# Kernel tuning notes

Hardware: AMD Instinct MI355X
Metric: run time of the kernel (lower is better)

The kernel has to match this reference:

```python
import jax, jax.numpy as jnp
import numpy as np

ALPHA = 0.2          # LeakyReLU negative slope
NEG = -9e15          # mask fill value, as in pyGAT GraphAttentionLayer
N, NIN, NHID, NOUT = 4096, 64, 32, 64
NHEADS, D_INT = 8, 32
H_INT = max(1, int(NHEADS * 0.25))   # 2 intent heads
H_SP = NHEADS - H_INT                # 6 spatial heads


def setup_inputs() -> dict:
    key = jax.random.key(0)
    ks = jax.random.split(key, 10)
    x = jax.random.normal(ks[0], (N, NIN), dtype=jnp.float32)
    adj = (jax.random.uniform(ks[1], (N, N)) < 0.01).astype(jnp.float32)
    adj = jnp.clip(adj + jnp.eye(N, dtype=jnp.float32), 0.0, 1.0)
    intent_embeds = jax.random.normal(ks[2], (N, D_INT), dtype=jnp.float32)
    # learned params (xavier-ish scale)
    def xav(k, shape):
        fan = shape[-2] if len(shape) > 1 else shape[-1]
        return jax.random.normal(k, shape, dtype=jnp.float32) / np.sqrt(fan)
    W_sp = xav(ks[3], (H_SP, NIN, NHID))       # spatial head projections
    a_sp = xav(ks[4], (H_SP, 2 * NHID))        # spatial attention vectors
    W_int = xav(ks[5], (H_INT, NIN, NHID))     # intent head projections
    a_int = xav(ks[6], (H_INT, 2 * D_INT))     # intent attention vectors (over intent embeds)
    W_out = xav(ks[7], (NHID * NHEADS, NOUT))  # output GAT layer
    a_out = xav(ks[8], (2 * NOUT,))
    return {"x": x, "adj": adj, "intent_embeds": intent_embeds,
            "W_sp": W_sp, "a_sp": a_sp, "W_int": W_int, "a_int": a_int,
            "W_out": W_out, "a_out": a_out}


def _masked_attend(e, mask, Wh):
    # e: [H,N,N] raw scores, mask: [1,N,N] bool, Wh: [H,N,F]
    att = jax.nn.softmax(jnp.where(mask, e, NEG), axis=-1)
    return jnp.einsum('hij,hjf->hif', att, Wh)


def reference(x, adj, intent_embeds, W_sp, a_sp, W_int, a_int, W_out, a_out):
    mask = (adj > 0)[None]                                   # [1,N,N]
    # ---- spatial heads (standard GAT, batched over heads) ----
    Wh_s = jnp.einsum('nf,hfo->hno', x, W_sp)                # [Hs,N,nhid]
    f1 = jnp.einsum('hno,ho->hn', Wh_s, a_sp[:, :NHID])
    f2 = jnp.einsum('hno,ho->hn', Wh_s, a_sp[:, NHID:])
    e_s = jax.nn.leaky_relu(f1[:, :, None] + f2[:, None, :], ALPHA)
    h_s = jax.nn.elu(_masked_attend(e_s, mask, Wh_s))        # concat=True -> elu
    # ---- intent heads: scores from intent embeddings, values from Wh ----
    Wh_i = jnp.einsum('nf,hfo->hno', x, W_int)               # [Hi,N,nhid]
    g1 = jnp.einsum('nd,hd->hn', intent_embeds, a_int[:, :D_INT])
    g2 = jnp.einsum('nd,hd->hn', intent_embeds, a_int[:, D_INT:])
    e_i = jax.nn.leaky_relu(g1[:, :, None] + g2[:, None, :], ALPHA)
    h_i = jax.nn.elu(_masked_attend(e_i, mask, Wh_i))        # [Hi,N,nhid]
    # ---- concat heads along feature dim: [N, nheads*nhid] ----
    h = jnp.concatenate([h_s, h_i], axis=0).transpose(1, 0, 2).reshape(N, -1)
    # ---- output attention layer (concat=False: no elu) ----
    Who = h @ W_out                                          # [N,nout]
    o1 = Who @ a_out[:NOUT]
    o2 = Who @ a_out[NOUT:]
    e_o = jax.nn.leaky_relu(o1[:, None] + o2[None, :], ALPHA)
    att_o = jax.nn.softmax(jnp.where(mask[0], e_o, NEG), axis=-1)
    out = att_o @ Who
    return jnp.tanh(out)
```

## Files before the change

kernel.cpp:

```cpp
#include <hip/hip_runtime.h>

#define N      4096
#define NIN    64
#define NHID   32
#define NOUT   64
#define NHEADS 8
#define H_SP   6
#define D_INT  32
#define MAXDEG 128
#define NPB    4
#define NPB2   2
#define ALPHA  0.2f

__device__ __forceinline__ int mbcnt64(unsigned long long m) {
    return __builtin_amdgcn_mbcnt_hi((unsigned)(m >> 32),
           __builtin_amdgcn_mbcnt_lo((unsigned)m, 0u));
}

__global__ __launch_bounds__(256) void k_fused1(
    const float* __restrict__ x, const float* __restrict__ ie,
    const float4* __restrict__ adj4,
    const float* __restrict__ Wsp, const float* __restrict__ asp,
    const float* __restrict__ Wint, const float* __restrict__ aint,
    float* __restrict__ Wh_t, float* __restrict__ src, float* __restrict__ dst_t,
    int* __restrict__ col, int* __restrict__ deg)
{
    const int nb   = blockIdx.x * NPB;
    const int tid  = threadIdx.x;
    const int wv   = tid >> 6, lane = tid & 63;
    const int h    = tid >> 5, f    = tid & 31;

    __shared__ float xs_t[NIN][NPB];
    __shared__ float ies[NPB][D_INT];

    xs_t[tid & 63][tid >> 6] = x[nb * NIN + tid];
    if (tid < NPB * D_INT) ies[tid >> 5][tid & 31] = ie[nb * D_INT + tid];
    __syncthreads();

    const float* W = (h < H_SP) ? (Wsp + h * NIN * NHID)
                                : (Wint + (h - H_SP) * NIN * NHID);
    float acc[NPB] = {0.f, 0.f, 0.f, 0.f};
#pragma unroll
    for (int c = 0; c < NIN; ++c) {
        const float wval = W[c * NHID + f];
        const float4 xv  = *(const float4*)&xs_t[c][0];
        acc[0] += xv.x * wval; acc[1] += xv.y * wval;
        acc[2] += xv.z * wval; acc[3] += xv.w * wval;
    }
#pragma unroll
    for (int m = 0; m < NPB; ++m)
        Wh_t[(size_t)(nb + m) * 256 + tid] = acc[m];

    const float a1v = (h < H_SP) ? asp[h * 64 + f]      : aint[(h - H_SP) * 64 + f];
    const float a2v = (h < H_SP) ? asp[h * 64 + 32 + f] : aint[(h - H_SP) * 64 + 32 + f];
#pragma unroll
    for (int m = 0; m < NPB; ++m) {
        const float b = (h < H_SP) ? acc[m] : ies[m][f];
        float s1 = b * a1v, s2 = b * a2v;
#pragma unroll
        for (int mm = 16; mm >= 1; mm >>= 1) {
            s1 += __shfl_xor(s1, mm);
            s2 += __shfl_xor(s2, mm);
        }
        if (f == 0) { src[h * N + nb + m] = s1; dst_t[(nb + m) * 8 + h] = s2; }
    }

    const int r = nb + wv;
    const float4* row = adj4 + (size_t)r * (N / 4);
    int cnt = 0;
#pragma unroll 4
    for (int t = 0; t < 16; ++t) {
        float4 v = row[t * 64 + lane];
        unsigned long long bx = __ballot(v.x > 0.f);
        unsigned long long by = __ballot(v.y > 0.f);
        unsigned long long bz = __ballot(v.z > 0.f);
        unsigned long long bw = __ballot(v.w > 0.f);
        const int tx = __popcll(bx), ty = __popcll(by);
        const int tz = __popcll(bz), tw = __popcll(bw);
        const int idx0 = (t * 64 + lane) * 4;
        const int px = cnt + mbcnt64(bx);
        const int py = cnt + tx + mbcnt64(by);
        const int pz = cnt + tx + ty + mbcnt64(bz);
        const int pw = cnt + tx + ty + tz + mbcnt64(bw);
        if (v.x > 0.f && px < MAXDEG) col[r * MAXDEG + px] = idx0;
        if (v.y > 0.f && py < MAXDEG) col[r * MAXDEG + py] = idx0 + 1;
        if (v.z > 0.f && pz < MAXDEG) col[r * MAXDEG + pz] = idx0 + 2;
        if (v.w > 0.f && pw < MAXDEG) col[r * MAXDEG + pw] = idx0 + 3;
        cnt += tx + ty + tz + tw;
    }
    if (lane == 0) deg[r] = (cnt < MAXDEG) ? cnt : MAXDEG;
}

__global__ __launch_bounds__(256) void k_attn1who(
    const int* __restrict__ col, const int* __restrict__ deg,
    const float* __restrict__ Wh_t, const float* __restrict__ src,
    const float* __restrict__ dst_t, const float* __restrict__ Wout,
    const float* __restrict__ aout,
    float* __restrict__ Who, float* __restrict__ o1, float* __restrict__ o2)
{
    const int r0  = blockIdx.x * NPB2;
    const int tid = threadIdx.x;
    const int h   = tid >> 5, lane = tid & 31;

    __shared__ int   cs[NPB2][MAXDEG];
    __shared__ float w[NPB2][NHEADS][MAXDEG];
    __shared__ float hs[NPB2][NHEADS * NHID];
    __shared__ float part[NPB2][4][NOUT];

    const int d0 = deg[r0], d1 = deg[r0 + 1];
    {
        const int m = tid >> 7, k = tid & 127;
        const int dm = m ? d1 : d0;
        cs[m][k] = (k < dm) ? col[(r0 + m) * MAXDEG + k] : 0;
    }
    __syncthreads();

#pragma unroll
    for (int m = 0; m < NPB2; ++m) {
        const int dm = m ? d1 : d0;
        const float sr = src[h * N + r0 + m];
        float ev[4];
        float mx = -3.4e38f;
#pragma unroll
        for (int t = 0; t < 4; ++t) {
            const int k = lane + t * 32;
            float e = -3.4e38f;
            if (k < dm) {
                e = sr + dst_t[cs[m][k] * 8 + h];
                e = e > 0.f ? e : ALPHA * e;
            }
            ev[t] = e;
            mx = fmaxf(mx, e);
        }
#pragma unroll
        for (int mm = 16; mm >= 1; mm >>= 1) mx = fmaxf(mx, __shfl_xor(mx, mm));
        float sum = 0.f;
#pragma unroll
        for (int t = 0; t < 4; ++t) {
            const int k = lane + t * 32;
            float p = (k < dm) ? __expf(ev[t] - mx) : 0.f;
            ev[t] = p;
            sum += p;
        }
#pragma unroll
        for (int mm = 16; mm >= 1; mm >>= 1) sum += __shfl_xor(sum, mm);
        const float inv = 1.f / sum;
#pragma unroll
        for (int t = 0; t < 4; ++t) w[m][h][lane + t * 32] = ev[t] * inv;
    }
    __syncthreads();

    const int d8a = (d0 + 7) & ~7, d8b = (d1 + 7) & ~7;
    const int d8m = d8a > d8b ? d8a : d8b;
    float a0 = 0.f, a1 = 0.f, c0 = 0.f, c1 = 0.f;
    for (int k = 0; k < d8m; k += 8) {
        int4   ja = *(const int4*)  &cs[0][k];
        int4   jA = *(const int4*)  &cs[0][k + 4];
        int4   jb = *(const int4*)  &cs[1][k];
        int4   jB = *(const int4*)  &cs[1][k + 4];
        float4 wa = *(const float4*)&w[0][h][k];
        float4 wA = *(const float4*)&w[0][h][k + 4];
        float4 wb = *(const float4*)&w[1][h][k];
        float4 wB = *(const float4*)&w[1][h][k + 4];
        a0 += wa.x * Wh_t[(size_t)ja.x * 256 + tid] + wa.y * Wh_t[(size_t)ja.y * 256 + tid]
            + wa.z * Wh_t[(size_t)ja.z * 256 + tid] + wa.w * Wh_t[(size_t)ja.w * 256 + tid];
        a1 += wA.x * Wh_t[(size_t)jA.x * 256 + tid] + wA.y * Wh_t[(size_t)jA.y * 256 + tid]
            + wA.z * Wh_t[(size_t)jA.z * 256 + tid] + wA.w * Wh_t[(size_t)jA.w * 256 + tid];
        c0 += wb.x * Wh_t[(size_t)jb.x * 256 + tid] + wb.y * Wh_t[(size_t)jb.y * 256 + tid]
            + wb.z * Wh_t[(size_t)jb.z * 256 + tid] + wb.w * Wh_t[(size_t)jb.w * 256 + tid];
        c1 += wB.x * Wh_t[(size_t)jB.x * 256 + tid] + wB.y * Wh_t[(size_t)jB.y * 256 + tid]
            + wB.z * Wh_t[(size_t)jB.z * 256 + tid] + wB.w * Wh_t[(size_t)jB.w * 256 + tid];
    }
    float av = a0 + a1; av = av > 0.f ? av : __expf(av) - 1.f;
    float cv = c0 + c1; cv = cv > 0.f ? cv : __expf(cv) - 1.f;
    hs[0][tid] = av;
    hs[1][tid] = cv;
    __syncthreads();

    const int fo = tid & 63, q = tid >> 6;
    float p0 = 0.f, p1 = 0.f;
#pragma unroll
    for (int c = q * 64; c < q * 64 + 64; ++c) {
        const float wv_ = Wout[c * NOUT + fo];
        p0 += hs[0][c] * wv_;
        p1 += hs[1][c] * wv_;
    }
    part[0][q][fo] = p0;
    part[1][q][fo] = p1;
    __syncthreads();

    if (tid < 128) {
        const int m = tid >> 6, fo2 = tid & 63;
        float who = part[m][0][fo2] + part[m][1][fo2] + part[m][2][fo2] + part[m][3][fo2];
        Who[(size_t)(r0 + m) * NOUT + fo2] = who;
        float v1 = who * aout[fo2];
        float v2 = who * aout[NOUT + fo2];
#pragma unroll
        for (int mm = 32; mm >= 1; mm >>= 1) {
            v1 += __shfl_xor(v1, mm);
            v2 += __shfl_xor(v2, mm);
        }
        if (fo2 == 0) { o1[r0 + m] = v1; o2[r0 + m] = v2; }
    }
}

__global__ __launch_bounds__(256) void k_attn2(
    const int* __restrict__ col, const int* __restrict__ deg,
    const float* __restrict__ Who, const float* __restrict__ o1,
    const float* __restrict__ o2, float* __restrict__ out)
{
    const int tid  = threadIdx.x;
    const int wv   = tid >> 6, lane = tid & 63;
    const int r    = blockIdx.x * 4 + wv;

    const int d  = deg[r];
    const int j0 = (lane < d)      ? col[r * MAXDEG + lane]      : 0;
    const int j1 = (lane + 64 < d) ? col[r * MAXDEG + 64 + lane] : 0;
    const float sr = o1[r];

    float e0 = -3.4e38f, e1 = -3.4e38f;
    if (lane < d)      { float e = sr + o2[j0]; e0 = e > 0.f ? e : ALPHA * e; }
    if (lane + 64 < d) { float e = sr + o2[j1]; e1 = e > 0.f ? e : ALPHA * e; }
    float mx = fmaxf(e0, e1);
#pragma unroll
    for (int m = 32; m >= 1; m >>= 1) mx = fmaxf(mx, __shfl_xor(mx, m));
    float p0 = (lane < d)      ? __expf(e0 - mx) : 0.f;
    float p1 = (lane + 64 < d) ? __expf(e1 - mx) : 0.f;
    float s = p0 + p1;
#pragma unroll
    for (int m = 32; m >= 1; m >>= 1) s += __shfl_xor(s, m);
    const float inv = 1.f / s;
    const float w0 = p0 * inv, w1 = p1 * inv;

    float acc = 0.f;
    const int dlo = d < 64 ? d : 64;
#pragma unroll 4
    for (int k = 0; k < dlo; ++k) {
        const int   j  = __builtin_amdgcn_readlane(j0, k);
        const float wt = __uint_as_float(
            __builtin_amdgcn_readlane(__float_as_uint(w0), k));
        acc += wt * Who[(size_t)j * NOUT + lane];
    }
#pragma unroll 2
    for (int k = 64; k < d; ++k) {
        const int   j  = __builtin_amdgcn_readlane(j1, k - 64);
        const float wt = __uint_as_float(
            __builtin_amdgcn_readlane(__float_as_uint(w1), k - 64));
        acc += wt * Who[(size_t)j * NOUT + lane];
    }
    out[(size_t)r * NOUT + lane] = tanhf(acc);
}

extern "C" void kernel_launch(void* const* d_in, const int* in_sizes, int n_in,
                              void* d_out, int out_size, void* d_ws, size_t ws_size,
                              hipStream_t stream) {
    const float* x    = (const float*)d_in[0];
    const float* adj  = (const float*)d_in[1];
    const float* ie   = (const float*)d_in[2];
    const float* Wsp  = (const float*)d_in[3];
    const float* asp  = (const float*)d_in[4];
    const float* Wint = (const float*)d_in[5];
    const float* aint = (const float*)d_in[6];
    const float* Wout = (const float*)d_in[7];
    const float* aout = (const float*)d_in[8];
    float* out = (float*)d_out;

    float* ws    = (float*)d_ws;
    float* Wh_t  = ws;
    float* src   = Wh_t + 1048576;
    float* dst_t = src  + 32768;
    float* Who   = dst_t + 32768;
    float* o1    = Who  + 262144;
    float* o2    = o1   + 4096;
    int*   col   = (int*)(o2 + 4096);
    int*   deg   = col + 4096 * MAXDEG;

    k_fused1  <<<N / NPB,  256, 0, stream>>>(x, ie, (const float4*)adj, Wsp, asp,
                                             Wint, aint, Wh_t, src, dst_t, col, deg);
    k_attn1who<<<N / NPB2, 256, 0, stream>>>(col, deg, Wh_t, src, dst_t, Wout, aout,
                                             Who, o1, o2);
    k_attn2   <<<N / 4,    256, 0, stream>>>(col, deg, Who, o1, o2, out);
}
```

Baseline: 170.3 us.

## Process one row per block and prefetch first neighbour gathers before softmax

The attention-aggregation kernel now handles one row per block instead of two, which doubles the grid and drops the padding to the longer row's degree. The first 16 neighbour feature gathers are issued right after the column indices land in shared memory, so their latency overlaps the softmax. The main loop is unrolled to 16 neighbours with four accumulators, and launch bounds ask for four blocks per CU. In exchange, each block now loads Wout on its own with no reuse across rows, and register pressure rises from the prefetched values.

```diff
diff --git a/kernel.cpp b/kernel.cpp
--- a/kernel.cpp
+++ b/kernel.cpp
@@ -9,7 +9,6 @@
 #define D_INT  32
 #define MAXDEG 128
 #define NPB    4
-#define NPB2   2
 #define ALPHA  0.2f
 
 __device__ __forceinline__ int mbcnt64(unsigned long long m) {
@@ -91,116 +90,143 @@
     if (lane == 0) deg[r] = (cnt < MAXDEG) ? cnt : MAXDEG;
 }
 
-__global__ __launch_bounds__(256) void k_attn1who(
+__global__ __launch_bounds__(256, 4) void k_attn1who(
     const int* __restrict__ col, const int* __restrict__ deg,
     const float* __restrict__ Wh_t, const float* __restrict__ src,
     const float* __restrict__ dst_t, const float* __restrict__ Wout,
     const float* __restrict__ aout,
     float* __restrict__ Who, float* __restrict__ o1, float* __restrict__ o2)
 {
-    const int r0  = blockIdx.x * NPB2;
+    const int r   = blockIdx.x;
     const int tid = threadIdx.x;
     const int h   = tid >> 5, lane = tid & 31;
 
-    __shared__ int   cs[NPB2][MAXDEG];
-    __shared__ float w[NPB2][NHEADS][MAXDEG];
-    __shared__ float hs[NPB2][NHEADS * NHID];
-    __shared__ float part[NPB2][4][NOUT];
-
-    const int d0 = deg[r0], d1 = deg[r0 + 1];
-    {
-        const int m = tid >> 7, k = tid & 127;
-        const int dm = m ? d1 : d0;
-        cs[m][k] = (k < dm) ? col[(r0 + m) * MAXDEG + k] : 0;
-    }
-    __syncthreads();
-
-#pragma unroll
-    for (int m = 0; m < NPB2; ++m) {
-        const int dm = m ? d1 : d0;
-        const float sr = src[h * N + r0 + m];
-        float ev[4];
-        float mx = -3.4e38f;
-#pragma unroll
-        for (int t = 0; t < 4; ++t) {
-            const int k = lane + t * 32;
-            float e = -3.4e38f;
-            if (k < dm) {
-                e = sr + dst_t[cs[m][k] * 8 + h];
-                e = e > 0.f ? e : ALPHA * e;
-            }
-            ev[t] = e;
-            mx = fmaxf(mx, e);
+    __shared__ __align__(16) int   cs[MAXDEG];
+    __shared__ __align__(16) float w[NHEADS][MAXDEG];
+    __shared__ float hs[NHEADS * NHID];
+    __shared__ float part[4][NOUT];
+
+    const int d = deg[r];
+    if (tid < MAXDEG) cs[tid] = (tid < d) ? col[r * MAXDEG + tid] : 0;
+    __syncthreads();
+
+    const int4 ja = *(const int4*)&cs[0];
+    const int4 jb = *(const int4*)&cs[4];
+    const int4 jc = *(const int4*)&cs[8];
+    const int4 jd = *(const int4*)&cs[12];
+    const float g0  = Wh_t[(size_t)ja.x * 256 + tid];
+    const float g1  = Wh_t[(size_t)ja.y * 256 + tid];
+    const float g2  = Wh_t[(size_t)ja.z * 256 + tid];
+    const float g3  = Wh_t[(size_t)ja.w * 256 + tid];
+    const float g4  = Wh_t[(size_t)jb.x * 256 + tid];
+    const float g5  = Wh_t[(size_t)jb.y * 256 + tid];
+    const float g6  = Wh_t[(size_t)jb.z * 256 + tid];
+    const float g7  = Wh_t[(size_t)jb.w * 256 + tid];
+    const float g8  = Wh_t[(size_t)jc.x * 256 + tid];
+    const float g9  = Wh_t[(size_t)jc.y * 256 + tid];
+    const float g10 = Wh_t[(size_t)jc.z * 256 + tid];
+    const float g11 = Wh_t[(size_t)jc.w * 256 + tid];
+    const float g12 = Wh_t[(size_t)jd.x * 256 + tid];
+    const float g13 = Wh_t[(size_t)jd.y * 256 + tid];
+    const float g14 = Wh_t[(size_t)jd.z * 256 + tid];
+    const float g15 = Wh_t[(size_t)jd.w * 256 + tid];
+
+    const float sr = src[h * N + r];
+    float ev[4];
+    float mx = -3.4e38f;
+#pragma unroll
+    for (int t = 0; t < 4; ++t) {
+        const int k = lane + t * 32;
+        float e = -3.4e38f;
+        if (k < d) {
+            e = sr + dst_t[cs[k] * 8 + h];
+            e = e > 0.f ? e : ALPHA * e;
         }
-#pragma unroll
-        for (int mm = 16; mm >= 1; mm >>= 1) mx = fmaxf(mx, __shfl_xor(mx, mm));
-        float sum = 0.f;
-#pragma unroll
-        for (int t = 0; t < 4; ++t) {
-            const int k = lane + t * 32;
-            float p = (k < dm) ? __expf(ev[t] - mx) : 0.f;
-            ev[t] = p;
-            sum += p;
+        ev[t] = e;
+        mx = fmaxf(mx, e);
+    }
+#pragma unroll
+    for (int mm = 16; mm >= 1; mm >>= 1) mx = fmaxf(mx, __shfl_xor(mx, mm));
+
+    float sum = 0.f;
+#pragma unroll
+    for (int t = 0; t < 4; ++t) {
+        const int k = lane + t * 32;
+        float p = (k < d) ? __expf(ev[t] - mx) : 0.f;
+        ev[t] = p;
+        sum += p;
+    }
+#pragma unroll
+    for (int mm = 16; mm >= 1; mm >>= 1) sum += __shfl_xor(sum, mm);
+    const float inv = 1.f / sum;
+#pragma unroll
+    for (int t = 0; t < 4; ++t)
+        w[h][lane + t * 32] = ev[t] * inv;
+    __syncthreads();
+
+    const float4 wa = *(const float4*)&w[h][0];
+    const float4 wb = *(const float4*)&w[h][4];
+    const float4 wc = *(const float4*)&w[h][8];
+    const float4 wd = *(const float4*)&w[h][12];
+    float acc0 = wa.x * g0  + wa.y * g1  + wa.z * g2  + wa.w * g3;
+    float acc1 = wb.x * g4  + wb.y * g5  + wb.z * g6  + wb.w * g7;
+    float acc2 = wc.x * g8  + wc.y * g9  + wc.z * g10 + wc.w * g11;
+    float acc3 = wd.x * g12 + wd.y * g13 + wd.z * g14 + wd.w * g15;
+
+    const int d16 = (d + 15) & ~15;
+    for (int k = 16; k < d16; k += 16) {
+        const int4 a = *(const int4*)&cs[k];
+        const int4 b = *(const int4*)&cs[k + 4];
+        const int4 c = *(const int4*)&cs[k + 8];
+        const int4 e = *(const int4*)&cs[k + 12];
+        const float4 w0 = *(const float4*)&w[h][k];
+        const float4 w1 = *(const float4*)&w[h][k + 4];
+        const float4 w2 = *(const float4*)&w[h][k + 8];
+        const float4 w3 = *(const float4*)&w[h][k + 12];
+        const float t0  = Wh_t[(size_t)a.x * 256 + tid];
+        const float t1  = Wh_t[(size_t)a.y * 256 + tid];
+        const float t2  = Wh_t[(size_t)a.z * 256 + tid];
+        const float t3  = Wh_t[(size_t)a.w * 256 + tid];
+        const float t4  = Wh_t[(size_t)b.x * 256 + tid];
+        const float t5  = Wh_t[(size_t)b.y * 256 + tid];
+        const float t6  = Wh_t[(size_t)b.z * 256 + tid];
+        const float t7  = Wh_t[(size_t)b.w * 256 + tid];
+        const float t8  = Wh_t[(size_t)c.x * 256 + tid];
+        const float t9  = Wh_t[(size_t)c.y * 256 + tid];
+        const float t10 = Wh_t[(size_t)c.z * 256 + tid];
+        const float t11 = Wh_t[(size_t)c.w * 256 + tid];
+        const float t12 = Wh_t[(size_t)e.x * 256 + tid];
+        const float t13 = Wh_t[(size_t)e.y * 256 + tid];
+        const float t14 = Wh_t[(size_t)e.z * 256 + tid];
+        const float t15 = Wh_t[(size_t)e.w * 256 + tid];
+        acc0 += w0.x * t0  + w0.y * t1  + w0.z * t2  + w0.w * t3;
+        acc1 += w1.x * t4  + w1.y * t5  + w1.z * t6  + w1.w * t7;
+        acc2 += w2.x * t8  + w2.y * t9  + w2.z * t10 + w2.w * t11;
+        acc3 += w3.x * t12 + w3.y * t13 + w3.z * t14 + w3.w * t15;
+    }
+    float acc = (acc0 + acc1) + (acc2 + acc3);
+    acc = acc > 0.f ? acc : __expf(acc) - 1.f;
+    hs[tid] = acc;
+    __syncthreads();
+
+    const int fo = tid & 63, q = tid >> 6;
+    float p = 0.f;
+#pragma unroll
+    for (int c = q * 64; c < q * 64 + 64; ++c) p += hs[c] * Wout[c * NOUT + fo];
+    part[q][fo] = p;
+    __syncthreads();
+
+    if (tid < 64) {
+        float who = part[0][tid] + part[1][tid] + part[2][tid] + part[3][tid];
+        Who[(size_t)r * NOUT + tid] = who;
+        float v1 = who * aout[tid];
+        float v2 = who * aout[NOUT + tid];
+#pragma unroll
+        for (int m = 32; m >= 1; m >>= 1) {
+            v1 += __shfl_xor(v1, m);
+            v2 += __shfl_xor(v2, m);
         }
-#pragma unroll
-        for (int mm = 16; mm >= 1; mm >>= 1) sum += __shfl_xor(sum, mm);
-        const float inv = 1.f / sum;
-#pragma unroll
-        for (int t = 0; t < 4; ++t) w[m][h][lane + t * 32] = ev[t] * inv;
-    }
-    __syncthreads();
-
-    const int d8a = (d0 + 7) & ~7, d8b = (d1 + 7) & ~7;
-    const int d8m = d8a > d8b ? d8a : d8b;
-    float a0 = 0.f, a1 = 0.f, c0 = 0.f, c1 = 0.f;
-    for (int k = 0; k < d8m; k += 8) {
-        int4   ja = *(const int4*)  &cs[0][k];
-        int4   jA = *(const int4*)  &cs[0][k + 4];
-        int4   jb = *(const int4*)  &cs[1][k];
-        int4   jB = *(const int4*)  &cs[1][k + 4];
-        float4 wa = *(const float4*)&w[0][h][k];
-        float4 wA = *(const float4*)&w[0][h][k + 4];
-        float4 wb = *(const float4*)&w[1][h][k];
-        float4 wB = *(const float4*)&w[1][h][k + 4];
-        a0 += wa.x * Wh_t[(size_t)ja.x * 256 + tid] + wa.y * Wh_t[(size_t)ja.y * 256 + tid]
-            + wa.z * Wh_t[(size_t)ja.z * 256 + tid] + wa.w * Wh_t[(size_t)ja.w * 256 + tid];
-        a1 += wA.x * Wh_t[(size_t)jA.x * 256 + tid] + wA.y * Wh_t[(size_t)jA.y * 256 + tid]
-            + wA.z * Wh_t[(size_t)jA.z * 256 + tid] + wA.w * Wh_t[(size_t)jA.w * 256 + tid];
-        c0 += wb.x * Wh_t[(size_t)jb.x * 256 + tid] + wb.y * Wh_t[(size_t)jb.y * 256 + tid]
-            + wb.z * Wh_t[(size_t)jb.z * 256 + tid] + wb.w * Wh_t[(size_t)jb.w * 256 + tid];
-        c1 += wB.x * Wh_t[(size_t)jB.x * 256 + tid] + wB.y * Wh_t[(size_t)jB.y * 256 + tid]
-            + wB.z * Wh_t[(size_t)jB.z * 256 + tid] + wB.w * Wh_t[(size_t)jB.w * 256 + tid];
-    }
-    float av = a0 + a1; av = av > 0.f ? av : __expf(av) - 1.f;
-    float cv = c0 + c1; cv = cv > 0.f ? cv : __expf(cv) - 1.f;
-    hs[0][tid] = av;
-    hs[1][tid] = cv;
-    __syncthreads();
-
-    const int fo = tid & 63, q = tid >> 6;
-    float p0 = 0.f, p1 = 0.f;
-#pragma unroll
-    for (int c = q * 64; c < q * 64 + 64; ++c) {
-        const float wv_ = Wout[c * NOUT + fo];
-        p0 += hs[0][c] * wv_;
-        p1 += hs[1][c] * wv_;
-    }
-    part[0][q][fo] = p0;
-    part[1][q][fo] = p1;
-    __syncthreads();
-
-    if (tid < 128) {
-        const int m = tid >> 6, fo2 = tid & 63;
-        float who = part[m][0][fo2] + part[m][1][fo2] + part[m][2][fo2] + part[m][3][fo2];
-        Who[(size_t)(r0 + m) * NOUT + fo2] = who;
-        float v1 = who * aout[fo2];
-        float v2 = who * aout[NOUT + fo2];
-#pragma unroll
-        for (int mm = 32; mm >= 1; mm >>= 1) {
-            v1 += __shfl_xor(v1, mm);
-            v2 += __shfl_xor(v2, mm);
-        }
-        if (fo2 == 0) { o1[r0 + m] = v1; o2[r0 + m] = v2; }
+        if (tid == 0) { o1[r] = v1; o2[r] = v2; }
     }
 }
 
@@ -275,9 +301,9 @@
     int*   col   = (int*)(o2 + 4096);
     int*   deg   = col + 4096 * MAXDEG;
 
-    k_fused1  <<<N / NPB,  256, 0, stream>>>(x, ie, (const float4*)adj, Wsp, asp,
-                                             Wint, aint, Wh_t, src, dst_t, col, deg);
-    k_attn1who<<<N / NPB2, 256, 0, stream>>>(col, deg, Wh_t, src, dst_t, Wout, aout,
-                                             Who, o1, o2);
-    k_attn2   <<<N / 4,    256, 0, stream>>>(col, deg, Who, o1, o2, out);
-}
+    k_fused1  <<<N / NPB, 256, 0, stream>>>(x, ie, (const float4*)adj, Wsp, asp,
+                                            Wint, aint, Wh_t, src, dst_t, col, deg);
+    k_attn1who<<<N,       256, 0, stream>>>(col, deg, Wh_t, src, dst_t, Wout, aout,
+                                            Who, o1, o2);
+    k_attn2   <<<N / 4,   256, 0, stream>>>(col, deg, Who, o1, o2, out);
+}
```

Result: faster. 159.0 us (-6.6%).

## Restructure attention kernel to one wave per row with all heads per lane

Applied to the files above, without the earlier changes.

Rewrites the middle attention+projection kernel so each 64-lane wave handles one row and every lane computes all 8 heads. The dst scores are loaded as float4 vectors and the softmax weights are stored head-interleaved in shared memory. Blocks grow to 8 rows and 512 threads, with Wout slices held in registers and reused across the 8 rows. The aim is fewer redundant dst_t loads and better Wout reuse, at the cost of higher register pressure and more shared memory per block.

```diff
diff --git a/kernel.cpp b/kernel.cpp
--- a/kernel.cpp
+++ b/kernel.cpp
@@ -9,7 +9,7 @@
 #define D_INT  32
 #define MAXDEG 128
 #define NPB    4
-#define NPB2   2
+#define ROWS   8
 #define ALPHA  0.2f
 
 __device__ __forceinline__ int mbcnt64(unsigned long long m) {
@@ -91,117 +91,145 @@
     if (lane == 0) deg[r] = (cnt < MAXDEG) ? cnt : MAXDEG;
 }
 
-__global__ __launch_bounds__(256) void k_attn1who(
+__global__ __launch_bounds__(512, 4) void k_attn1who(
     const int* __restrict__ col, const int* __restrict__ deg,
     const float* __restrict__ Wh_t, const float* __restrict__ src,
     const float* __restrict__ dst_t, const float* __restrict__ Wout,
     const float* __restrict__ aout,
     float* __restrict__ Who, float* __restrict__ o1, float* __restrict__ o2)
 {
-    const int r0  = blockIdx.x * NPB2;
-    const int tid = threadIdx.x;
-    const int h   = tid >> 5, lane = tid & 31;
-
-    __shared__ int   cs[NPB2][MAXDEG];
-    __shared__ float w[NPB2][NHEADS][MAXDEG];
-    __shared__ float hs[NPB2][NHEADS * NHID];
-    __shared__ float part[NPB2][4][NOUT];
-
-    const int d0 = deg[r0], d1 = deg[r0 + 1];
+    const int r0   = blockIdx.x * ROWS;
+    const int tid  = threadIdx.x;
+    const int wv   = tid >> 6, lane = tid & 63;
+    const int r    = r0 + wv;
+
+    __shared__ __align__(16) int   cs[ROWS][MAXDEG];
+    __shared__ __align__(16) float w_smem[ROWS * MAXDEG * NHEADS];
+    __shared__ __align__(16) float hs[ROWS][NHEADS * NHID];
+
+    const int d  = deg[r];
+    const int j0 = (lane < d)      ? col[r * MAXDEG + lane]      : 0;
+    const int j1 = (lane + 64 < d) ? col[r * MAXDEG + 64 + lane] : 0;
+    cs[wv][lane]      = (lane < d)      ? j0 : 0;
+    cs[wv][lane + 64] = (lane + 64 < d) ? j1 : 0;
+
+    float sr[NHEADS];
+#pragma unroll
+    for (int h = 0; h < NHEADS; ++h) sr[h] = src[h * N + r];
+
+    float dA[NHEADS] = {}, dB[NHEADS] = {};
+    if (lane < d) {
+        *(float4*)&dA[0] = *(const float4*)&dst_t[j0 * 8];
+        *(float4*)&dA[4] = *(const float4*)&dst_t[j0 * 8 + 4];
+    }
+    if (lane + 64 < d) {
+        *(float4*)&dB[0] = *(const float4*)&dst_t[j1 * 8];
+        *(float4*)&dB[4] = *(const float4*)&dst_t[j1 * 8 + 4];
+    }
+
+    float eA[NHEADS], eB[NHEADS], mx[NHEADS];
+#pragma unroll
+    for (int h = 0; h < NHEADS; ++h) {
+        float a = sr[h] + dA[h]; a = a > 0.f ? a : ALPHA * a;
+        float b = sr[h] + dB[h]; b = b > 0.f ? b : ALPHA * b;
+        eA[h] = (lane < d)      ? a : -3.4e38f;
+        eB[h] = (lane + 64 < d) ? b : -3.4e38f;
+        mx[h] = fmaxf(eA[h], eB[h]);
+    }
+#pragma unroll
+    for (int m = 32; m >= 1; m >>= 1)
+#pragma unroll
+        for (int h = 0; h < NHEADS; ++h) mx[h] = fmaxf(mx[h], __shfl_xor(mx[h], m));
+
+    float pA[NHEADS], pB[NHEADS], sum[NHEADS];
+#pragma unroll
+    for (int h = 0; h < NHEADS; ++h) {
+        pA[h] = (lane < d)      ? __expf(eA[h] - mx[h]) : 0.f;
+        pB[h] = (lane + 64 < d) ? __expf(eB[h] - mx[h]) : 0.f;
+        sum[h] = pA[h] + pB[h];
+    }
+#pragma unroll
+    for (int m = 32; m >= 1; m >>= 1)
+#pragma unroll
+        for (int h = 0; h < NHEADS; ++h) sum[h] += __shfl_xor(sum[h], m);
+
     {
-        const int m = tid >> 7, k = tid & 127;
-        const int dm = m ? d1 : d0;
-        cs[m][k] = (k < dm) ? col[(r0 + m) * MAXDEG + k] : 0;
-    }
+        float inv[NHEADS];
+#pragma unroll
+        for (int h = 0; h < NHEADS; ++h) inv[h] = 1.f / sum[h];
+        float* wa = &w_smem[(wv * MAXDEG + lane) * 8];
+        *(float4*)&wa[0] = make_float4(pA[0]*inv[0], pA[2]*inv[2], pA[4]*inv[4], pA[6]*inv[6]);
+        *(float4*)&wa[4] = make_float4(pA[1]*inv[1], pA[3]*inv[3], pA[5]*inv[5], pA[7]*inv[7]);
+        float* wb = &w_smem[(wv * MAXDEG + lane + 64) * 8];
+        *(float4*)&wb[0] = make_float4(pB[0]*inv[0], pB[2]*inv[2], pB[4]*inv[4], pB[6]*inv[6]);
+        *(float4*)&wb[4] = make_float4(pB[1]*inv[1], pB[3]*inv[3], pB[5]*inv[5], pB[7]*inv[7]);
+    }
+
+    const int d4 = (d + 3) & ~3;
+    const float* wrow = &w_smem[wv * MAXDEG * 8 + (lane >> 5) * 4];
+    const int*   csr_ = &cs[wv][0];
+    float a0 = 0.f, a1 = 0.f, a2 = 0.f, a3 = 0.f;
+    for (int k = 0; k < d4; k += 4) {
+        const int4 jj = *(const int4*)&csr_[k];
+        const float* p0 = Wh_t + (size_t)jj.x * 256 + lane;
+        const float* p1 = Wh_t + (size_t)jj.y * 256 + lane;
+        const float* p2 = Wh_t + (size_t)jj.z * 256 + lane;
+        const float* p3 = Wh_t + (size_t)jj.w * 256 + lane;
+        const float g00 = p0[0], g01 = p0[64], g02 = p0[128], g03 = p0[192];
+        const float g10 = p1[0], g11 = p1[64], g12 = p1[128], g13 = p1[192];
+        const float g20 = p2[0], g21 = p2[64], g22 = p2[128], g23 = p2[192];
+        const float g30 = p3[0], g31 = p3[64], g32 = p3[128], g33 = p3[192];
+        const float4 w0 = *(const float4*)&wrow[(k + 0) * 8];
+        const float4 w1 = *(const float4*)&wrow[(k + 1) * 8];
+        const float4 w2 = *(const float4*)&wrow[(k + 2) * 8];
+        const float4 w3 = *(const float4*)&wrow[(k + 3) * 8];
+        a0 += w0.x * g00 + w1.x * g10 + w2.x * g20 + w3.x * g30;
+        a1 += w0.y * g01 + w1.y * g11 + w2.y * g21 + w3.y * g31;
+        a2 += w0.z * g02 + w1.z * g12 + w2.z * g22 + w3.z * g32;
+        a3 += w0.w * g03 + w1.w * g13 + w2.w * g23 + w3.w * g33;
+    }
+    a0 = a0 > 0.f ? a0 : __expf(a0) - 1.f;
+    a1 = a1 > 0.f ? a1 : __expf(a1) - 1.f;
+    a2 = a2 > 0.f ? a2 : __expf(a2) - 1.f;
+    a3 = a3 > 0.f ? a3 : __expf(a3) - 1.f;
+    hs[wv][lane]       = a0;
+    hs[wv][lane + 64]  = a1;
+    hs[wv][lane + 128] = a2;
+    hs[wv][lane + 192] = a3;
     __syncthreads();
 
-#pragma unroll
-    for (int m = 0; m < NPB2; ++m) {
-        const int dm = m ? d1 : d0;
-        const float sr = src[h * N + r0 + m];
-        float ev[4];
-        float mx = -3.4e38f;
-#pragma unroll
-        for (int t = 0; t < 4; ++t) {
-            const int k = lane + t * 32;
-            float e = -3.4e38f;
-            if (k < dm) {
-                e = sr + dst_t[cs[m][k] * 8 + h];
-                e = e > 0.f ? e : ALPHA * e;
+    float* part = w_smem;
+    {
+        float wreg[32];
+#pragma unroll
+        for (int cc = 0; cc < 32; ++cc)
+            wreg[cc] = Wout[(wv * 32 + cc) * NOUT + lane];
+#pragma unroll
+        for (int m = 0; m < ROWS; ++m) {
+            float acc = 0.f;
+#pragma unroll
+            for (int cc = 0; cc < 32; cc += 4) {
+                const float4 hv = *(const float4*)&hs[m][wv * 32 + cc];
+                acc += hv.x * wreg[cc]     + hv.y * wreg[cc + 1]
+                     + hv.z * wreg[cc + 2] + hv.w * wreg[cc + 3];
             }
-            ev[t] = e;
-            mx = fmaxf(mx, e);
+            part[(wv * ROWS + m) * NOUT + lane] = acc;
         }
-#pragma unroll
-        for (int mm = 16; mm >= 1; mm >>= 1) mx = fmaxf(mx, __shfl_xor(mx, mm));
-        float sum = 0.f;
-#pragma unroll
-        for (int t = 0; t < 4; ++t) {
-            const int k = lane + t * 32;
-            float p = (k < dm) ? __expf(ev[t] - mx) : 0.f;
-            ev[t] = p;
-            sum += p;
-        }
-#pragma unroll
-        for (int mm = 16; mm >= 1; mm >>= 1) sum += __shfl_xor(sum, mm);
-        const float inv = 1.f / sum;
-#pragma unroll
-        for (int t = 0; t < 4; ++t) w[m][h][lane + t * 32] = ev[t] * inv;
     }
     __syncthreads();
 
-    const int d8a = (d0 + 7) & ~7, d8b = (d1 + 7) & ~7;
-    const int d8m = d8a > d8b ? d8a : d8b;
-    float a0 = 0.f, a1 = 0.f, c0 = 0.f, c1 = 0.f;
-    for (int k = 0; k < d8m; k += 8) {
-        int4   ja = *(const int4*)  &cs[0][k];
-        int4   jA = *(const int4*)  &cs[0][k + 4];
-        int4   jb = *(const int4*)  &cs[1][k];
-        int4   jB = *(const int4*)  &cs[1][k + 4];
-        float4 wa = *(const float4*)&w[0][h][k];
-        float4 wA = *(const float4*)&w[0][h][k + 4];
-        float4 wb = *(const float4*)&w[1][h][k];
-        float4 wB = *(const float4*)&w[1][h][k + 4];
-        a0 += wa.x * Wh_t[(size_t)ja.x * 256 + tid] + wa.y * Wh_t[(size_t)ja.y * 256 + tid]
-            + wa.z * Wh_t[(size_t)ja.z * 256 + tid] + wa.w * Wh_t[(size_t)ja.w * 256 + tid];
-        a1 += wA.x * Wh_t[(size_t)jA.x * 256 + tid] + wA.y * Wh_t[(size_t)jA.y * 256 + tid]
-            + wA.z * Wh_t[(size_t)jA.z * 256 + tid] + wA.w * Wh_t[(size_t)jA.w * 256 + tid];
-        c0 += wb.x * Wh_t[(size_t)jb.x * 256 + tid] + wb.y * Wh_t[(size_t)jb.y * 256 + tid]
-            + wb.z * Wh_t[(size_t)jb.z * 256 + tid] + wb.w * Wh_t[(size_t)jb.w * 256 + tid];
-        c1 += wB.x * Wh_t[(size_t)jB.x * 256 + tid] + wB.y * Wh_t[(size_t)jB.y * 256 + tid]
-            + wB.z * Wh_t[(size_t)jB.z * 256 + tid] + wB.w * Wh_t[(size_t)jB.w * 256 + tid];
-    }
-    float av = a0 + a1; av = av > 0.f ? av : __expf(av) - 1.f;
-    float cv = c0 + c1; cv = cv > 0.f ? cv : __expf(cv) - 1.f;
-    hs[0][tid] = av;
-    hs[1][tid] = cv;
-    __syncthreads();
-
-    const int fo = tid & 63, q = tid >> 6;
-    float p0 = 0.f, p1 = 0.f;
-#pragma unroll
-    for (int c = q * 64; c < q * 64 + 64; ++c) {
-        const float wv_ = Wout[c * NOUT + fo];
-        p0 += hs[0][c] * wv_;
-        p1 += hs[1][c] * wv_;
-    }
-    part[0][q][fo] = p0;
-    part[1][q][fo] = p1;
-    __syncthreads();
-
-    if (tid < 128) {
-        const int m = tid >> 6, fo2 = tid & 63;
-        float who = part[m][0][fo2] + part[m][1][fo2] + part[m][2][fo2] + part[m][3][fo2];
-        Who[(size_t)(r0 + m) * NOUT + fo2] = who;
-        float v1 = who * aout[fo2];
-        float v2 = who * aout[NOUT + fo2];
-#pragma unroll
-        for (int mm = 32; mm >= 1; mm >>= 1) {
-            v1 += __shfl_xor(v1, mm);
-            v2 += __shfl_xor(v2, mm);
-        }
-        if (fo2 == 0) { o1[r0 + m] = v1; o2[r0 + m] = v2; }
-    }
+    float who = 0.f;
+#pragma unroll
+    for (int q = 0; q < 8; ++q) who += part[(q * ROWS + wv) * NOUT + lane];
+    Who[(size_t)r * NOUT + lane] = who;
+    float v1 = who * aout[lane];
+    float v2 = who * aout[NOUT + lane];
+#pragma unroll
+    for (int m = 32; m >= 1; m >>= 1) {
+        v1 += __shfl_xor(v1, m);
+        v2 += __shfl_xor(v2, m);
+    }
+    if (lane == 0) { o1[r] = v1; o2[r] = v2; }
 }
 
 __global__ __launch_bounds__(256) void k_attn2(
@@ -277,7 +305,7 @@
 
     k_fused1  <<<N / NPB,  256, 0, stream>>>(x, ie, (const float4*)adj, Wsp, asp,
                                              Wint, aint, Wh_t, src, dst_t, col, deg);
-    k_attn1who<<<N / NPB2, 256, 0, stream>>>(col, deg, Wh_t, src, dst_t, Wout, aout,
+    k_attn1who<<<N / ROWS, 512, 0, stream>>>(col, deg, Wh_t, src, dst_t, Wout, aout,
                                              Who, o1, o2);
     k_attn2   <<<N / 4,    256, 0, stream>>>(col, deg, Who, o1, o2, out);
 }
```

After: 150.4 us. 1.13x faster.
